# Kernel tuning notes

Measured on AMD Instinct MI355X. Metric: run time of the kernel, lower is better.

The kernel has to match this reference:

```python
import jax, jax.numpy as jnp
import numpy as np

B, L, H = 4, 1024, 8192
NH, HD = 64, 128
PD = HD // 2  # 64, rope-style positional dim
QL = HD * 4 * 3  # 1536, Q latent dim
KVL = HD * 4     # 512, KV latent dim


def setup_inputs() -> dict:
    key = jax.random.key(0)
    ks = jax.random.split(key, 18)
    w = lambda k, i, o: (jax.random.normal(k, (i, o), jnp.float32) * (1.0 / np.sqrt(i))).astype(jnp.float32)
    b = lambda k, o: jnp.zeros((o,), jnp.float32)
    return {
        'x': jax.random.normal(ks[0], (B, L, H), jnp.float32),
        'W_dq': w(ks[1], H, QL),   'b_dq': b(ks[2], QL),
        'W_dkv': w(ks[3], H, KVL), 'b_dkv': b(ks[4], KVL),
        'W_uq': w(ks[5], QL, H),   'b_uq': b(ks[6], H),
        'W_uk': w(ks[7], KVL, H),  'b_uk': b(ks[8], H),
        'W_uv': w(ks[9], KVL, H),  'b_uv': b(ks[10], H),
        'W_pq': w(ks[11], QL, NH * PD), 'b_pq': b(ks[12], NH * PD),
        'W_pk': w(ks[13], H, PD),  'b_pk': b(ks[14], PD),
        'W_o': w(ks[15], H, H),    'b_o': b(ks[16], H),
    }


def reference(x, W_dq, b_dq, W_dkv, b_dkv, W_uq, b_uq, W_uk, b_uk,
              W_uv, b_uv, W_pq, b_pq, W_pk, b_pk, W_o, b_o):
    Bb, Ll, Hh = x.shape
    # low-rank latents
    Q_lat = x @ W_dq + b_dq          # (B, L, 1536)
    KV_lat = x @ W_dkv + b_dkv       # (B, L, 512)
    # up-projections
    Q_c = (Q_lat @ W_uq + b_uq).reshape(Bb, Ll, NH, HD)
    Q_r = (Q_lat @ W_pq + b_pq).reshape(Bb, Ll, NH, PD)
    Q = jnp.concatenate([Q_c, Q_r], axis=-1)            # (B, L, NH, 192)
    K_c = (KV_lat @ W_uk + b_uk).reshape(Bb, Ll, NH, HD)
    K_r = x @ W_pk + b_pk                                # (B, L, 64), shared across heads
    K_r = jnp.broadcast_to(K_r[:, :, None, :], (Bb, Ll, NH, PD))
    K = jnp.concatenate([K_c, K_r], axis=-1)             # (B, L, NH, 192)
    V = (KV_lat @ W_uv + b_uv).reshape(Bb, Ll, NH, HD)   # (B, L, NH, 128)
    # attention with mismatched Q/K (192) vs V (128) head dims; scale by sqrt(128)
    scores = jnp.einsum('bqhd,bkhd->bhqk', Q, K) / np.float32(np.sqrt(HD))
    causal = jnp.tril(jnp.ones((Ll, Ll), bool))
    scores = jnp.where(causal, scores, jnp.float32(-jnp.inf))
    attn = jax.nn.softmax(scores, axis=-1)               # dropout = identity (eval)
    out = jnp.einsum('bhqk,bkhd->bqhd', attn, V).reshape(Bb, Ll, Hh)
    return out @ W_o + b_o
```

## Files before the change

kernel.cpp:

```cpp
#include <hip/hip_runtime.h>
#include <cstdint>

typedef unsigned short u16;
typedef __attribute__((ext_vector_type(8))) short bf16x8;
typedef __attribute__((ext_vector_type(4))) float f32x4;
typedef __attribute__((ext_vector_type(4))) unsigned short u16x4;

__device__ __forceinline__ u16 f2b(float f) {
  union { float f; uint32_t u; } v; v.f = f;
  uint32_t r = v.u + 0x7FFFu + ((v.u >> 16) & 1u);
  return (u16)(r >> 16);
}

__device__ __forceinline__ void gload_lds16(const void* g, void* l) {
  __builtin_amdgcn_global_load_lds((const __attribute__((address_space(1))) void*)g,
                                   (__attribute__((address_space(3))) void*)l, 16, 0, 0);
}

__device__ __forceinline__ void barrier_raw() {
  __builtin_amdgcn_sched_barrier(0);
  asm volatile("" ::: "memory");
  __builtin_amdgcn_s_barrier();
  asm volatile("" ::: "memory");
  __builtin_amdgcn_sched_barrier(0);
}
__device__ __forceinline__ void wait_vm8() {
  asm volatile("s_waitcnt vmcnt(8)" ::: "memory");
  __builtin_amdgcn_sched_barrier(0);
}

__global__ __launch_bounds__(256) void cvt_bf16(const float* __restrict__ in,
                                                u16* __restrict__ out, long n) {
  long i = ((long)blockIdx.x * 256 + threadIdx.x) * 4;
  if (i >= n) return;
  f32x4 v = *(const f32x4*)(in + i);
  u16x4 o;
#pragma unroll
  for (int k = 0; k < 4; k++) o[k] = f2b(v[k]);
  *(u16x4*)(out + i) = o;
}

__global__ __launch_bounds__(256) void transpose_cvt(const float* __restrict__ W,
                                                     u16* __restrict__ WT, int K, int N) {
  __shared__ float tile[32][33];
  const int tn0 = blockIdx.x * 32;
  const int tk0 = blockIdx.y * 32;
  const int c = threadIdx.x & 31;
  const int r0 = threadIdx.x >> 5;
#pragma unroll
  for (int rr = 0; rr < 32; rr += 8)
    tile[r0 + rr][c] = W[(long)(tk0 + r0 + rr) * N + tn0 + c];
  __syncthreads();
#pragma unroll
  for (int rr = 0; rr < 32; rr += 8)
    WT[(long)(tn0 + r0 + rr) * K + tk0 + c] = f2b(tile[c][r0 + rr]);
}

__global__ __launch_bounds__(256) void biascat3(const float* __restrict__ a,
                                                const float* __restrict__ b,
                                                const float* __restrict__ c,
                                                float* __restrict__ o) {
  int i = blockIdx.x * 256 + threadIdx.x;
  if (i < 1536) o[i] = a[i];
  else if (i < 2048) o[i] = b[i - 1536];
  else if (i < 2112) o[i] = c[i - 2048];
}
__global__ __launch_bounds__(256) void biascat2(const float* __restrict__ a,
                                                const float* __restrict__ b,
                                                int na, int n, float* __restrict__ o) {
  int i = blockIdx.x * 256 + threadIdx.x;
  if (i >= n) return;
  o[i] = (i < na) ? a[i] : b[i - na];
}

__global__ __launch_bounds__(256) void repl_kr(const u16* __restrict__ Kr,
                                               u16* __restrict__ Kbuf, int stride) {
  long idx = (long)blockIdx.x * 256 + threadIdx.x;
  int d4 = idx & 15;
  long t = idx >> 4;
  int hh = t & 63;
  long tok = t >> 6;
  if (tok >= 4096) return;
  u16x4 v = *(const u16x4*)(Kr + tok * (long)stride + d4 * 4);
  long b = tok >> 10, l = tok & 1023;
  *(u16x4*)(Kbuf + ((b * 64 + hh) * 1024 + l) * 192 + 128 + d4 * 4) = v;
}

template<int MODE>
__global__ __launch_bounds__(512, 2) void gemm256(
    const u16* __restrict__ A, long lda, const u16* __restrict__ BT,
    const float* __restrict__ bias, void* __restrict__ outp, void* __restrict__ outp2,
    int N, int K) {
  __shared__ u16 sA[2][2][8192];
  __shared__ u16 sB[2][2][8192];
  const int tid = threadIdx.x;
  const int lane = tid & 63;
  const int w = tid >> 6;
  const int wr = w >> 2, wc = w & 3;
  const int hi = lane >> 4, lo = lane & 15;

  const int Nt = gridDim.x, Mt = gridDim.y;
  const int bid = blockIdx.y * Nt + blockIdx.x;
  const int xcd = bid & 7;
  const int idx = bid >> 3;
  int mt, nt;
  if ((Nt & 1) == 0) {
    const int Rm = Mt >> 2, Rn = Nt >> 1;
    const int xr = xcd & 3, xcn = xcd >> 2;
    const int Wb = Rn < 8 ? Rn : 8;
    const int cb = idx / (Rm * Wb);
    const int rem = idx - cb * (Rm * Wb);
    mt = xr * Rm + (rem % Rm);
    nt = xcn * Rn + cb * Wb + rem / Rm;
  } else {
    const int Rm = Mt >> 3;
    const int Wb = Nt < 8 ? Nt : 8;
    const int cb = idx / (Rm * Wb);
    const int rem = idx - cb * (Rm * Wb);
    mt = xcd * Rm + (rem % Rm);
    nt = cb * Wb + rem / Rm;
  }
  const long m0 = (long)mt * 256;
  const long n0 = (long)nt * 256;

  const int nkt = K >> 6;

  const int srow = tid >> 2;
  const int scol = ((tid & 3) ^ ((tid >> 3) & 3)) * 8;
  const long arow0 = m0 + srow, arow1 = arow0 + 128;
  long brow0 = n0 + srow, brow1 = brow0 + 128;
  if (brow0 > N - 1) brow0 = N - 1;
  if (brow1 > N - 1) brow1 = N - 1;
  const u16* aS0 = A + arow0 * lda + scol;
  const u16* aS1 = A + arow1 * lda + scol;
  const u16* bS0 = BT + brow0 * (long)K + scol;
  const u16* bS1 = BT + brow1 * (long)K + scol;

  const int aRd = (wr * 128 + lo) * 32 + (hi ^ ((lo >> 1) & 3)) * 8;
  const int bRd = (wc * 64 + lo) * 32 + (hi ^ ((lo >> 1) & 3)) * 8;

  f32x4 acc[8][4] = {};

#define STAGE(s0, s1, koff, dst) do { \
    gload_lds16((s0) + (koff), (dst) + tid * 8); \
    gload_lds16((s1) + (koff), (dst) + 4096 + tid * 8); \
  } while (0)
#define LDA_F(bufr, kh, m) (*(const bf16x8*)(&sA[bufr][kh][aRd + (m) * 512]))
#define LDB_F(bufr, kh, n) (*(const bf16x8*)(&sB[bufr][kh][bRd + (n) * 512]))
#define MFMA_GRP(mi, av) \
    acc[mi][0] = __builtin_amdgcn_mfma_f32_16x16x32_bf16(av, b0, acc[mi][0], 0, 0, 0); \
    acc[mi][1] = __builtin_amdgcn_mfma_f32_16x16x32_bf16(av, b1, acc[mi][1], 0, 0, 0); \
    acc[mi][2] = __builtin_amdgcn_mfma_f32_16x16x32_bf16(av, b2, acc[mi][2], 0, 0, 0); \
    acc[mi][3] = __builtin_amdgcn_mfma_f32_16x16x32_bf16(av, b3, acc[mi][3], 0, 0, 0);

  STAGE(aS0, aS1, 0, &sA[0][0][0]);
  STAGE(bS0, bS1, 0, &sB[0][0][0]);
  STAGE(aS0, aS1, 32, &sA[0][1][0]);
  STAGE(bS0, bS1, 32, &sB[0][1][0]);
  {
    const long t1o = (nkt > 1) ? 64 : 0;
    STAGE(aS0, aS1, t1o, &sA[1][0][0]);
    STAGE(bS0, bS1, t1o, &sB[1][0][0]);
  }
  wait_vm8();
  barrier_raw();

  for (int t = 0; t < nkt; ++t) {
    const int cur = t & 1, nxt = cur ^ 1;
    const int t1c = (t + 1 < nkt) ? t + 1 : nkt - 1;
    const int t2c = (t + 2 < nkt) ? t + 2 : nkt - 1;
    const long o1 = (long)t1c * 64;
    const long o2 = (long)t2c * 64;
    bf16x8 b0, b1, b2, b3, a0, a1, a2, a3, a4, a5, a6, a7;
    b0 = LDB_F(cur, 0, 0); b1 = LDB_F(cur, 0, 1); b2 = LDB_F(cur, 0, 2); b3 = LDB_F(cur, 0, 3);
    a0 = LDA_F(cur, 0, 0); a1 = LDA_F(cur, 0, 1); a2 = LDA_F(cur, 0, 2); a3 = LDA_F(cur, 0, 3);
    a4 = LDA_F(cur, 0, 4); a5 = LDA_F(cur, 0, 5); a6 = LDA_F(cur, 0, 6); a7 = LDA_F(cur, 0, 7);
    STAGE(aS0, aS1, o1 + 32, &sA[nxt][1][0]);
    barrier_raw();
    __builtin_amdgcn_s_setprio(1);
    MFMA_GRP(0, a0) MFMA_GRP(1, a1) MFMA_GRP(2, a2) MFMA_GRP(3, a3)
    __builtin_amdgcn_s_setprio(0);
    STAGE(bS0, bS1, o1 + 32, &sB[nxt][1][0]);
    __builtin_amdgcn_s_setprio(1);
    MFMA_GRP(4, a4) MFMA_GRP(5, a5) MFMA_GRP(6, a6) MFMA_GRP(7, a7)
    __builtin_amdgcn_s_setprio(0);
    wait_vm8();
    barrier_raw();
    b0 = LDB_F(cur, 1, 0); b1 = LDB_F(cur, 1, 1); b2 = LDB_F(cur, 1, 2); b3 = LDB_F(cur, 1, 3);
    a0 = LDA_F(cur, 1, 0); a1 = LDA_F(cur, 1, 1); a2 = LDA_F(cur, 1, 2); a3 = LDA_F(cur, 1, 3);
    a4 = LDA_F(cur, 1, 4); a5 = LDA_F(cur, 1, 5); a6 = LDA_F(cur, 1, 6); a7 = LDA_F(cur, 1, 7);
    STAGE(aS0, aS1, o2, &sA[cur][0][0]);
    barrier_raw();
    __builtin_amdgcn_s_setprio(1);
    MFMA_GRP(0, a0) MFMA_GRP(1, a1) MFMA_GRP(2, a2) MFMA_GRP(3, a3)
    __builtin_amdgcn_s_setprio(0);
    STAGE(bS0, bS1, o2, &sB[cur][0][0]);
    __builtin_amdgcn_s_setprio(1);
    MFMA_GRP(4, a4) MFMA_GRP(5, a5) MFMA_GRP(6, a6) MFMA_GRP(7, a7)
    __builtin_amdgcn_s_setprio(0);
    wait_vm8();
    barrier_raw();
  }
  asm volatile("s_waitcnt vmcnt(0)" ::: "memory");

#undef STAGE
#undef LDA_F
#undef LDB_F
#undef MFMA_GRP

#pragma unroll
  for (int m = 0; m < 8; m++) {
#pragma unroll
    for (int n = 0; n < 4; n++) {
      const long mb = m0 + wr * 128 + m * 16 + hi * 4;
      const long nn = n0 + wc * 64 + n * 16 + lo;
      if (nn >= N) continue;
      const float bv = bias[nn];
      if (MODE == 0) {
#pragma unroll
        for (int r = 0; r < 4; r++)
          ((u16*)outp)[(mb + r) * (long)N + nn] = f2b(acc[m][n][r] + bv);
      } else if (MODE == 3) {
#pragma unroll
        for (int r = 0; r < 4; r++)
          ((float*)outp)[(mb + r) * (long)N + nn] = acc[m][n][r] + bv;
      } else if (MODE == 4) {
        if (nn < 8192) {
          const long h = nn >> 7, d = nn & 127;
#pragma unroll
          for (int r = 0; r < 4; r++) {
            const long mm = mb + r;
            const long bq = mm >> 10, l = mm & 1023;
            ((u16*)outp)[((bq * 64 + h) * 1024 + l) * 192 + d] = f2b(acc[m][n][r] + bv);
          }
        } else {
          const long q = nn - 8192;
          const long h = q >> 6, d = q & 63;
#pragma unroll
          for (int r = 0; r < 4; r++) {
            const long mm = mb + r;
            const long bq = mm >> 10, l = mm & 1023;
            ((u16*)outp)[((bq * 64 + h) * 1024 + l) * 192 + 128 + d] = f2b(acc[m][n][r] + bv);
          }
        }
      } else {
        if (nn < 8192) {
          const long h = nn >> 7, d = nn & 127;
#pragma unroll
          for (int r = 0; r < 4; r++) {
            const long mm = mb + r;
            const long bq = mm >> 10, l = mm & 1023;
            ((u16*)outp)[((bq * 64 + h) * 1024 + l) * 192 + d] = f2b(acc[m][n][r] + bv);
          }
        } else {
          const long v = nn - 8192;
          const long h = v >> 7, d = v & 127;
          u16x4 pk;
#pragma unroll
          for (int r = 0; r < 4; r++) pk[r] = f2b(acc[m][n][r] + bv);
          const long bq = mb >> 10, l = mb & 1023;
          *(u16x4*)((u16*)outp2 + ((bq * 64 + h) * 128 + d) * 1024 + l) = pk;
        }
      }
    }
  }
}

__global__ __launch_bounds__(512, 2) void attn256(const u16* __restrict__ Qb,
                                                  const u16* __restrict__ Kb,
                                                  const u16* __restrict__ Vt,
                                                  u16* __restrict__ O) {
  __shared__ u16 sK[2][12288];
  __shared__ u16 sV[2][8192];
  __shared__ u16 P[8][32][72];
  const int bh = blockIdx.x;
  const int qtb = 3 - blockIdx.y;
  const int b = bh >> 6, h = bh & 63;
  const int tid = threadIdx.x, w = tid >> 6, lane = tid & 63;
  const int hi = lane >> 4, lo = lane & 15, lo7 = lane & 7;
  const int q0w = qtb * 256 + w * 32;
  const u16* Qh = Qb + (size_t)bh * 1024 * 192;
  const u16* Kh = Kb + (size_t)bh * 1024 * 192;
  const u16* Vh = Vt + (size_t)bh * 128 * 1024;
  const float scale = 0.08838834764831845f;
  const float NEGINF = -3.0e38f;

  int kOff0, kOff1, kOff2, vOff0, vOff1;
  {
    int g0 = tid, g1 = tid + 512, g2 = tid + 1024;
    int r0 = g0 / 24, r1 = g1 / 24, r2 = g2 / 24;
    kOff0 = r0 * 192 + ((g0 - r0 * 24) ^ (r0 & 7)) * 8;
    kOff1 = r1 * 192 + ((g1 - r1 * 24) ^ (r1 & 7)) * 8;
    kOff2 = r2 * 192 + ((g2 - r2 * 24) ^ (r2 & 7)) * 8;
    int s0 = tid, s1 = tid + 512;
    vOff0 = (s0 >> 3) * 1024 + ((s0 & 7) ^ ((s0 >> 3) & 7)) * 8;
    vOff1 = (s1 >> 3) * 1024 + ((s1 & 7) ^ ((s1 >> 3) & 7)) * 8;
  }
#define STAGE_KV(tt, bb) do { \
    const u16* kb_ = Kh + (size_t)(tt) * (64 * 192); \
    const u16* vb_ = Vh + (size_t)(tt) * 64; \
    gload_lds16(kb_ + kOff0, &sK[bb][0] + tid * 8); \
    gload_lds16(kb_ + kOff1, &sK[bb][4096] + tid * 8); \
    gload_lds16(kb_ + kOff2, &sK[bb][8192] + tid * 8); \
    gload_lds16(vb_ + vOff0, &sV[bb][0] + tid * 8); \
    gload_lds16(vb_ + vOff1, &sV[bb][4096] + tid * 8); \
  } while (0)

  bf16x8 qf[2][6];
#pragma unroll
  for (int qi = 0; qi < 2; qi++) {
    const u16* qp = Qh + (size_t)(q0w + qi * 16 + lo) * 192 + hi * 8;
#pragma unroll
    for (int f = 0; f < 6; f++) qf[qi][f] = *(const bf16x8*)(qp + f * 32);
  }

  f32x4 oacc[2][8] = {};
  float m_run[2][4], l_run[2][4];
#pragma unroll
  for (int qi = 0; qi < 2; qi++)
#pragma unroll
    for (int r = 0; r < 4; r++) { m_run[qi][r] = NEGINF; l_run[qi][r] = 0.f; }

  const int nkt = (qtb + 1) * 4;
  STAGE_KV(0, 0);
  __syncthreads();

  for (int t = 0; t < nkt; t++) {
    const int cur = t & 1;
    const int tn = (t + 1 < nkt) ? t + 1 : nkt - 1;
    STAGE_KV(tn, cur ^ 1);
    const int k0 = t * 64;
    if (k0 < q0w + 32) {
      f32x4 s[2][4] = {};
      __builtin_amdgcn_s_setprio(1);
#pragma unroll
      for (int j = 0; j < 4; j++) {
#pragma unroll
        for (int f = 0; f < 6; f++) {
          bf16x8 kf = *(const bf16x8*)(&sK[cur][((j * 16 + lo) * 24 + ((f * 4 + hi) ^ lo7)) * 8]);
          s[0][j] = __builtin_amdgcn_mfma_f32_16x16x32_bf16(qf[0][f], kf, s[0][j], 0, 0, 0);
          s[1][j] = __builtin_amdgcn_mfma_f32_16x16x32_bf16(qf[1][f], kf, s[1][j], 0, 0, 0);
        }
      }
      __builtin_amdgcn_s_setprio(0);
      const bool diag = (k0 + 63 > q0w);
#pragma unroll
      for (int qi = 0; qi < 2; qi++) {
#pragma unroll
        for (int r = 0; r < 4; r++) {
          const int q = q0w + qi * 16 + hi * 4 + r;
          float sv[4];
          float mx = NEGINF;
#pragma unroll
          for (int j = 0; j < 4; j++) {
            float v = s[qi][j][r] * scale;
            if (diag && (k0 + j * 16 + lo > q)) v = NEGINF;
            sv[j] = v;
            mx = fmaxf(mx, v);
          }
#pragma unroll
          for (int o = 1; o < 16; o <<= 1) mx = fmaxf(mx, __shfl_xor(mx, o, 64));
          const float mnew = fmaxf(m_run[qi][r], mx);
          float sum = 0.f;
#pragma unroll
          for (int j = 0; j < 4; j++) {
            float pv = __expf(sv[j] - mnew);
            sum += pv;
            P[w][qi * 16 + hi * 4 + r][j * 16 + lo] = f2b(pv);
          }
#pragma unroll
          for (int o = 1; o < 16; o <<= 1) sum += __shfl_xor(sum, o, 64);
          const float alpha = __expf(m_run[qi][r] - mnew);
          l_run[qi][r] = l_run[qi][r] * alpha + sum;
          m_run[qi][r] = mnew;
#pragma unroll
          for (int j = 0; j < 8; j++) oacc[qi][j][r] *= alpha;
        }
      }
      __builtin_amdgcn_s_setprio(1);
#pragma unroll
      for (int kk = 0; kk < 2; kk++) {
        bf16x8 pf0 = *(const bf16x8*)(&P[w][lo][kk * 32 + hi * 8]);
        bf16x8 pf1 = *(const bf16x8*)(&P[w][16 + lo][kk * 32 + hi * 8]);
#pragma unroll
        for (int j = 0; j < 8; j++) {
          bf16x8 vf = *(const bf16x8*)(&sV[cur][((j * 16 + lo) * 8 + ((kk * 4 + hi) ^ lo7)) * 8]);
          oacc[0][j] = __builtin_amdgcn_mfma_f32_16x16x32_bf16(pf0, vf, oacc[0][j], 0, 0, 0);
          oacc[1][j] = __builtin_amdgcn_mfma_f32_16x16x32_bf16(pf1, vf, oacc[1][j], 0, 0, 0);
        }
      }
      __builtin_amdgcn_s_setprio(0);
    }
    __syncthreads();
  }
#undef STAGE_KV

#pragma unroll
  for (int qi = 0; qi < 2; qi++) {
#pragma unroll
    for (int r = 0; r < 4; r++) {
      const float inv = 1.f / l_run[qi][r];
      const int q = q0w + qi * 16 + hi * 4 + r;
      u16* op = O + ((size_t)(b * 1024 + q) * 64 + h) * 128;
#pragma unroll
      for (int j = 0; j < 8; j++)
        op[j * 16 + lo] = f2b(oacc[qi][j][r] * inv);
    }
  }
}

extern "C" void kernel_launch(void* const* d_in, const int* in_sizes, int n_in,
                              void* d_out, int out_size, void* d_ws, size_t ws_size,
                              hipStream_t stream) {
  const float* x     = (const float*)d_in[0];
  const float* W_dq  = (const float*)d_in[1];
  const float* b_dq  = (const float*)d_in[2];
  const float* W_dkv = (const float*)d_in[3];
  const float* b_dkv = (const float*)d_in[4];
  const float* W_uq  = (const float*)d_in[5];
  const float* b_uq  = (const float*)d_in[6];
  const float* W_uk  = (const float*)d_in[7];
  const float* b_uk  = (const float*)d_in[8];
  const float* W_uv  = (const float*)d_in[9];
  const float* b_uv  = (const float*)d_in[10];
  const float* W_pq  = (const float*)d_in[11];
  const float* b_pq  = (const float*)d_in[12];
  const float* W_pk  = (const float*)d_in[13];
  const float* b_pk  = (const float*)d_in[14];
  const float* W_o   = (const float*)d_in[15];
  const float* b_o   = (const float*)d_in[16];

  char* ws = (char*)d_ws;
  size_t off = 0;
  auto alloc = [&](size_t bytes) {
    char* p = ws + off;
    off += (bytes + 255) & ~(size_t)255;
    return p;
  };
  u16* xbf   = (u16*)alloc(33554432ULL * 2);
  u16* WT    = (u16*)alloc(67108864ULL * 2);
  u16* lat   = (u16*)alloc(4096ULL * 2112 * 2);
  float* bct = (float*)alloc(2112ULL * 4);
  float* bq  = (float*)alloc(12288ULL * 4);
  float* bkv = (float*)alloc(16384ULL * 4);
  u16* Qbuf  = (u16*)alloc(100663296ULL);
  u16* Kbuf  = (u16*)alloc(100663296ULL);
  u16* Vt    = (u16*)alloc(67108864ULL);
  u16* Obuf  = xbf;
  if (off > ws_size) return;

  dim3 blk(256), blk5(512);
  cvt_bf16<<<dim3(32768), blk, 0, stream>>>(x, xbf, 33554432L);
  transpose_cvt<<<dim3(48, 256), blk, 0, stream>>>(W_dq, WT, 8192, 1536);
  transpose_cvt<<<dim3(16, 256), blk, 0, stream>>>(W_dkv, WT + 1536L * 8192, 8192, 512);
  transpose_cvt<<<dim3(2, 256), blk, 0, stream>>>(W_pk, WT + 2048L * 8192, 8192, 64);
  biascat3<<<dim3(9), blk, 0, stream>>>(b_dq, b_dkv, b_pk, bct);
  gemm256<0><<<dim3(9, 16), blk5, 0, stream>>>(xbf, 8192, WT, bct, lat, nullptr, 2112, 8192);
  repl_kr<<<dim3(16384), blk, 0, stream>>>(lat + 2048, Kbuf, 2112);
  transpose_cvt<<<dim3(256, 48), blk, 0, stream>>>(W_uq, WT, 1536, 8192);
  transpose_cvt<<<dim3(128, 48), blk, 0, stream>>>(W_pq, WT + 8192L * 1536, 1536, 4096);
  biascat2<<<dim3(48), blk, 0, stream>>>(b_uq, b_pq, 8192, 12288, bq);
  gemm256<4><<<dim3(48, 16), blk5, 0, stream>>>(lat, 2112, WT, bq, Qbuf, nullptr, 12288, 1536);
  transpose_cvt<<<dim3(256, 16), blk, 0, stream>>>(W_uk, WT, 512, 8192);
  transpose_cvt<<<dim3(256, 16), blk, 0, stream>>>(W_uv, WT + 8192L * 512, 512, 8192);
  biascat2<<<dim3(64), blk, 0, stream>>>(b_uk, b_uv, 8192, 16384, bkv);
  gemm256<5><<<dim3(64, 16), blk5, 0, stream>>>(lat + 1536, 2112, WT, bkv, Kbuf, Vt, 16384, 512);
  attn256<<<dim3(256, 4), blk5, 0, stream>>>(Qbuf, Kbuf, Vt, Obuf);
  transpose_cvt<<<dim3(256, 256), blk, 0, stream>>>(W_o, WT, 8192, 8192);
  gemm256<3><<<dim3(32, 16), blk5, 0, stream>>>(Obuf, 8192, WT, b_o, d_out, nullptr, 8192, 8192);
}
```

Baseline: 1.381 ms.

## Fuse weight prep into one launch and shrink attention to 128-query blocks

```diff
diff --git a/kernel.cpp b/kernel.cpp
--- a/kernel.cpp
+++ b/kernel.cpp
@@ -29,15 +29,48 @@
   __builtin_amdgcn_sched_barrier(0);
 }
 
-__global__ __launch_bounds__(256) void cvt_bf16(const float* __restrict__ in,
-                                                u16* __restrict__ out, long n) {
-  long i = ((long)blockIdx.x * 256 + threadIdx.x) * 4;
-  if (i >= n) return;
-  f32x4 v = *(const f32x4*)(in + i);
-  u16x4 o;
-#pragma unroll
-  for (int k = 0; k < 4; k++) o[k] = f2b(v[k]);
-  *(u16x4*)(out + i) = o;
+struct PJobs {
+  const float* s[7];
+  int K[7];
+  int N[7];
+  long off[7];
+  int cum[7];
+};
+
+__global__ __launch_bounds__(256) void prep(PJobs J, const float* __restrict__ x,
+                                            u16* __restrict__ xbf, u16* __restrict__ WT) {
+  const int bid = blockIdx.x;
+  if (bid < 32768) {
+    long i = ((long)bid * 256 + threadIdx.x) * 4;
+    f32x4 v = *(const f32x4*)(x + i);
+    u16x4 o;
+#pragma unroll
+    for (int k = 0; k < 4; k++) o[k] = f2b(v[k]);
+    *(u16x4*)(xbf + i) = o;
+    return;
+  }
+  __shared__ float tile[32][33];
+  const int tb = bid - 32768;
+  int j = 0;
+#pragma unroll
+  for (int t = 0; t < 6; t++) if (tb >= J.cum[t]) j = t + 1;
+  const int base = j ? J.cum[j - 1] : 0;
+  const int lt = tb - base;
+  const int K = J.K[j], N = J.N[j];
+  const float* W = J.s[j];
+  u16* dst = WT + J.off[j];
+  const int nb = N >> 5;
+  const int tn0 = (lt % nb) * 32;
+  const int tk0 = (lt / nb) * 32;
+  const int c = threadIdx.x & 31;
+  const int r0 = threadIdx.x >> 5;
+#pragma unroll
+  for (int rr = 0; rr < 32; rr += 8)
+    tile[r0 + rr][c] = W[(long)(tk0 + r0 + rr) * N + tn0 + c];
+  __syncthreads();
+#pragma unroll
+  for (int rr = 0; rr < 32; rr += 8)
+    dst[(long)(tn0 + r0 + rr) * K + tk0 + c] = f2b(tile[c][r0 + rr]);
 }
 
 __global__ __launch_bounds__(256) void transpose_cvt(const float* __restrict__ W,
@@ -88,7 +121,7 @@
 
 template<int MODE>
 __global__ __launch_bounds__(512, 2) void gemm256(
-    const u16* __restrict__ A, long lda, const u16* __restrict__ BT,
+    const u16* __restrict__ A, long lda, const u16* __restrict__ BT, long ldb,
     const float* __restrict__ bias, void* __restrict__ outp, void* __restrict__ outp2,
     int N, int K) {
   __shared__ u16 sA[2][2][8192];
@@ -133,8 +166,8 @@
   if (brow1 > N - 1) brow1 = N - 1;
   const u16* aS0 = A + arow0 * lda + scol;
   const u16* aS1 = A + arow1 * lda + scol;
-  const u16* bS0 = BT + brow0 * (long)K + scol;
-  const u16* bS1 = BT + brow1 * (long)K + scol;
+  const u16* bS0 = BT + brow0 * ldb + scol;
+  const u16* bS1 = BT + brow1 * ldb + scol;
 
   const int aRd = (wr * 128 + lo) * 32 + (hi ^ ((lo >> 1) & 3)) * 8;
   const int bRd = (wc * 64 + lo) * 32 + (hi ^ ((lo >> 1) & 3)) * 8;
@@ -266,44 +299,36 @@
   }
 }
 
-__global__ __launch_bounds__(512, 2) void attn256(const u16* __restrict__ Qb,
+__global__ __launch_bounds__(256, 2) void attn128(const u16* __restrict__ Qb,
                                                   const u16* __restrict__ Kb,
                                                   const u16* __restrict__ Vt,
                                                   u16* __restrict__ O) {
   __shared__ u16 sK[2][12288];
-  __shared__ u16 sV[2][8192];
-  __shared__ u16 P[8][32][72];
+  __shared__ u16 P[4][32][64];
   const int bh = blockIdx.x;
-  const int qtb = 3 - blockIdx.y;
+  const int qtb = 7 - blockIdx.y;
   const int b = bh >> 6, h = bh & 63;
   const int tid = threadIdx.x, w = tid >> 6, lane = tid & 63;
   const int hi = lane >> 4, lo = lane & 15, lo7 = lane & 7;
-  const int q0w = qtb * 256 + w * 32;
+  const int q0w = qtb * 128 + w * 32;
   const u16* Qh = Qb + (size_t)bh * 1024 * 192;
   const u16* Kh = Kb + (size_t)bh * 1024 * 192;
   const u16* Vh = Vt + (size_t)bh * 128 * 1024;
   const float scale = 0.08838834764831845f;
   const float NEGINF = -3.0e38f;
 
-  int kOff0, kOff1, kOff2, vOff0, vOff1;
-  {
-    int g0 = tid, g1 = tid + 512, g2 = tid + 1024;
-    int r0 = g0 / 24, r1 = g1 / 24, r2 = g2 / 24;
-    kOff0 = r0 * 192 + ((g0 - r0 * 24) ^ (r0 & 7)) * 8;
-    kOff1 = r1 * 192 + ((g1 - r1 * 24) ^ (r1 & 7)) * 8;
-    kOff2 = r2 * 192 + ((g2 - r2 * 24) ^ (r2 & 7)) * 8;
-    int s0 = tid, s1 = tid + 512;
-    vOff0 = (s0 >> 3) * 1024 + ((s0 & 7) ^ ((s0 >> 3) & 7)) * 8;
-    vOff1 = (s1 >> 3) * 1024 + ((s1 & 7) ^ ((s1 >> 3) & 7)) * 8;
-  }
-#define STAGE_KV(tt, bb) do { \
+  int kOff[6];
+#pragma unroll
+  for (int c = 0; c < 6; c++) {
+    int g = tid + 256 * c;
+    int row = g / 24;
+    kOff[c] = row * 192 + ((g - row * 24) ^ (row & 7)) * 8;
+  }
+#define STAGE_K(tt, bb) do { \
     const u16* kb_ = Kh + (size_t)(tt) * (64 * 192); \
-    const u16* vb_ = Vh + (size_t)(tt) * 64; \
-    gload_lds16(kb_ + kOff0, &sK[bb][0] + tid * 8); \
-    gload_lds16(kb_ + kOff1, &sK[bb][4096] + tid * 8); \
-    gload_lds16(kb_ + kOff2, &sK[bb][8192] + tid * 8); \
-    gload_lds16(vb_ + vOff0, &sV[bb][0] + tid * 8); \
-    gload_lds16(vb_ + vOff1, &sV[bb][4096] + tid * 8); \
+    _Pragma("unroll") \
+    for (int c = 0; c < 6; c++) \
+      gload_lds16(kb_ + kOff[c], &sK[bb][0] + (size_t)(tid + 256 * c) * 8); \
   } while (0)
 
   bf16x8 qf[2][6];
@@ -321,14 +346,14 @@
 #pragma unroll
     for (int r = 0; r < 4; r++) { m_run[qi][r] = NEGINF; l_run[qi][r] = 0.f; }
 
-  const int nkt = (qtb + 1) * 4;
-  STAGE_KV(0, 0);
+  const int nkt = 2 * qtb + 2;
+  STAGE_K(0, 0);
   __syncthreads();
 
   for (int t = 0; t < nkt; t++) {
     const int cur = t & 1;
     const int tn = (t + 1 < nkt) ? t + 1 : nkt - 1;
-    STAGE_KV(tn, cur ^ 1);
+    STAGE_K(tn, cur ^ 1);
     const int k0 = t * 64;
     if (k0 < q0w + 32) {
       f32x4 s[2][4] = {};
@@ -349,6 +374,7 @@
 #pragma unroll
         for (int r = 0; r < 4; r++) {
           const int q = q0w + qi * 16 + hi * 4 + r;
+          const int row = qi * 16 + hi * 4 + r;
           float sv[4];
           float mx = NEGINF;
 #pragma unroll
@@ -366,7 +392,7 @@
           for (int j = 0; j < 4; j++) {
             float pv = __expf(sv[j] - mnew);
             sum += pv;
-            P[w][qi * 16 + hi * 4 + r][j * 16 + lo] = f2b(pv);
+            P[w][row][((2 * j + (lo >> 3)) ^ (row & 7)) * 8 + (lo & 7)] = f2b(pv);
           }
 #pragma unroll
           for (int o = 1; o < 16; o <<= 1) sum += __shfl_xor(sum, o, 64);
@@ -380,11 +406,11 @@
       __builtin_amdgcn_s_setprio(1);
 #pragma unroll
       for (int kk = 0; kk < 2; kk++) {
-        bf16x8 pf0 = *(const bf16x8*)(&P[w][lo][kk * 32 + hi * 8]);
-        bf16x8 pf1 = *(const bf16x8*)(&P[w][16 + lo][kk * 32 + hi * 8]);
+        bf16x8 pf0 = *(const bf16x8*)(&P[w][lo][((kk * 4 + hi) ^ lo7) * 8]);
+        bf16x8 pf1 = *(const bf16x8*)(&P[w][16 + lo][((kk * 4 + hi) ^ lo7) * 8]);
 #pragma unroll
         for (int j = 0; j < 8; j++) {
-          bf16x8 vf = *(const bf16x8*)(&sV[cur][((j * 16 + lo) * 8 + ((kk * 4 + hi) ^ lo7)) * 8]);
+          bf16x8 vf = *(const bf16x8*)(Vh + (size_t)(j * 16 + lo) * 1024 + k0 + kk * 32 + hi * 8);
           oacc[0][j] = __builtin_amdgcn_mfma_f32_16x16x32_bf16(pf0, vf, oacc[0][j], 0, 0, 0);
           oacc[1][j] = __builtin_amdgcn_mfma_f32_16x16x32_bf16(pf1, vf, oacc[1][j], 0, 0, 0);
         }
@@ -393,7 +419,7 @@
     }
     __syncthreads();
   }
-#undef STAGE_KV
+#undef STAGE_K
 
 #pragma unroll
   for (int qi = 0; qi < 2; qi++) {
@@ -449,23 +475,31 @@
   u16* Obuf  = xbf;
   if (off > ws_size) return;
 
+  const long QOFF   = 2112L * 8192;
+  const long KVOFF2 = QOFF + 12288L * 1536;
+
   dim3 blk(256), blk5(512);
-  cvt_bf16<<<dim3(32768), blk, 0, stream>>>(x, xbf, 33554432L);
-  transpose_cvt<<<dim3(48, 256), blk, 0, stream>>>(W_dq, WT, 8192, 1536);
-  transpose_cvt<<<dim3(16, 256), blk, 0, stream>>>(W_dkv, WT + 1536L * 8192, 8192, 512);
-  transpose_cvt<<<dim3(2, 256), blk, 0, stream>>>(W_pk, WT + 2048L * 8192, 8192, 64);
+  {
+    PJobs J;
+    J.s[0] = W_dq;  J.K[0] = 8192; J.N[0] = 1536; J.off[0] = 0;
+    J.s[1] = W_dkv; J.K[1] = 8192; J.N[1] = 512;  J.off[1] = 1536L * 8192;
+    J.s[2] = W_pk;  J.K[2] = 8192; J.N[2] = 64;   J.off[2] = 2048L * 8192;
+    J.s[3] = W_uq;  J.K[3] = 1536; J.N[3] = 8192; J.off[3] = QOFF;
+    J.s[4] = W_pq;  J.K[4] = 1536; J.N[4] = 4096; J.off[4] = QOFF + 8192L * 1536;
+    J.s[5] = W_uk;  J.K[5] = 512;  J.N[5] = 8192; J.off[5] = KVOFF2;
+    J.s[6] = W_uv;  J.K[6] = 512;  J.N[6] = 8192; J.off[6] = KVOFF2 + 8192L * 512;
+    J.cum[0] = 12288; J.cum[1] = 16384; J.cum[2] = 16896; J.cum[3] = 29184;
+    J.cum[4] = 35328; J.cum[5] = 39424; J.cum[6] = 43520;
+    prep<<<dim3(32768 + 43520), blk, 0, stream>>>(J, x, xbf, WT);
+  }
   biascat3<<<dim3(9), blk, 0, stream>>>(b_dq, b_dkv, b_pk, bct);
-  gemm256<0><<<dim3(9, 16), blk5, 0, stream>>>(xbf, 8192, WT, bct, lat, nullptr, 2112, 8192);
+  biascat2<<<dim3(48), blk, 0, stream>>>(b_uq, b_pq, 8192, 12288, bq);
+  biascat2<<<dim3(64), blk, 0, stream>>>(b_uk, b_uv, 8192, 16384, bkv);
+  gemm256<0><<<dim3(9, 16), blk5, 0, stream>>>(xbf, 8192, WT, 8192, bct, lat, nullptr, 2112, 8192);
   repl_kr<<<dim3(16384), blk, 0, stream>>>(lat + 2048, Kbuf, 2112);
-  transpose_cvt<<<dim3(256, 48), blk, 0, stream>>>(W_uq, WT, 1536, 8192);
-  transpose_cvt<<<dim3(128, 48), blk, 0, stream>>>(W_pq, WT + 8192L * 1536, 1536, 4096);
-  biascat2<<<dim3(48), blk, 0, stream>>>(b_uq, b_pq, 8192, 12288, bq);
-  gemm256<4><<<dim3(48, 16), blk5, 0, stream>>>(lat, 2112, WT, bq, Qbuf, nullptr, 12288, 1536);
-  transpose_cvt<<<dim3(256, 16), blk, 0, stream>>>(W_uk, WT, 512, 8192);
-  transpose_cvt<<<dim3(256, 16), blk, 0, stream>>>(W_uv, WT + 8192L * 512, 512, 8192);
-  biascat2<<<dim3(64), blk, 0, stream>>>(b_uk, b_uv, 8192, 16384, bkv);
-  gemm256<5><<<dim3(64, 16), blk5, 0, stream>>>(lat + 1536, 2112, WT, bkv, Kbuf, Vt, 16384, 512);
-  attn256<<<dim3(256, 4), blk5, 0, stream>>>(Qbuf, Kbuf, Vt, Obuf);
+  gemm256<4><<<dim3(48, 16), blk5, 0, stream>>>(lat, 2112, WT + QOFF, 1536, bq, Qbuf, nullptr, 12288, 1536);
+  gemm256<5><<<dim3(64, 16), blk5, 0, stream>>>(lat + 1536, 2112, WT + KVOFF2, 512, bkv, Kbuf, Vt, 16384, 512);
+  attn128<<<dim3(256, 8), blk, 0, stream>>>(Qbuf, Kbuf, Vt, Obuf);
   transpose_cvt<<<dim3(256, 256), blk, 0, stream>>>(W_o, WT, 8192, 8192);
-  gemm256<3><<<dim3(32, 16), blk5, 0, stream>>>(Obuf, 8192, WT, b_o, d_out, nullptr, 8192, 8192);
-}
+  gemm256<3><<<dim3(32, 16), blk5, 0, stream>>>(Obuf, 8192, WT, 8192, b_o, d_out, nullptr, 8192, 8192);
+}
```

After: 1.532 ms. 1.11x slower.
